# Optimization experiments

Measured on AMD Instinct MI355X. Metric: run time of the kernel, lower is better.

The kernel has to match this reference:

```python
import jax, jax.numpy as jnp
import numpy as np

NEG_SLOPE = 0.01  # torch LeakyReLU default

def leaky_relu(x):
    return jnp.where(x >= 0, x, NEG_SLOPE * x)

def setup_inputs() -> dict:
    key = jax.random.key(0)
    ks = jax.random.split(key, 12)
    D = 128
    N_U, N_I, E = 100000, 50000, 1000000
    s = 1.0 / np.sqrt(D)
    return {
        "h_user": jax.random.normal(ks[0], (N_U, D), jnp.float32),
        "h_item": jax.random.normal(ks[1], (N_I, D), jnp.float32),
        "src_idx": jax.random.randint(ks[2], (E,), 0, N_U, jnp.int64) if jax.config.jax_enable_x64 else jax.random.randint(ks[2], (E,), 0, N_U, jnp.int32),
        "dst_idx": jax.random.randint(ks[3], (E,), 0, N_I, jnp.int32),
        "W_left": jax.random.normal(ks[4], (D, D), jnp.float32) * s,
        "b_left": jax.random.normal(ks[5], (D,), jnp.float32) * s,
        "W_right": jax.random.normal(ks[6], (D, D), jnp.float32) * s,
        "b_right": jax.random.normal(ks[7], (D,), jnp.float32) * s,
        "W1": jax.random.normal(ks[8], (D, D), jnp.float32) * s,
        "b1": jax.random.normal(ks[9], (D,), jnp.float32) * s,
        "W2": jax.random.normal(ks[10], (D, 1), jnp.float32) * s,
        "b2": jax.random.normal(ks[11], (1,), jnp.float32) * s,
    }

def reference(h_user, h_item, src_idx, dst_idx,
              W_left, b_left, W_right, b_right, W1, b1, W2, b2):
    # node linear transforms (dropout is identity in eval mode)
    u_f = h_user @ W_left + b_left      # [N_u, D]
    i_f = h_item @ W_right + b_right    # [N_i, D]
    # edge gather + add (dgl fn.u_add_v)
    score = u_f[src_idx] + i_f[dst_idx]  # [E, D]
    # pred MLP: LeakyReLU -> Linear(D,D) -> LeakyReLU -> Linear(D,1) -> LeakyReLU
    x = leaky_relu(score)
    x = leaky_relu(x @ W1 + b1)
    x = leaky_relu(x @ W2 + b2)         # [E, 1]
    return x
```

## Files before the change

kernel.cpp:

```cpp
#include <hip/hip_runtime.h>

typedef __attribute__((ext_vector_type(8))) short bf16x8;
typedef __attribute__((ext_vector_type(4))) float f32x4;
typedef __attribute__((ext_vector_type(2))) float f32x2;

__device__ __forceinline__ float leaky(float v) { return fmaxf(v, 0.01f * v); }

__device__ __forceinline__ unsigned short f2bf(float a) {
    unsigned int u = __float_as_uint(a);
    return (unsigned short)((u + 0x7FFFu + ((u >> 16) & 1u)) >> 16);
}

__device__ __forceinline__ unsigned int cvtpk(float a, float b) {
#if __has_builtin(__builtin_amdgcn_cvt_pk_bf16_f32)
    typedef __attribute__((ext_vector_type(2))) __bf16 bf2_t;
    bf2_t v = __builtin_amdgcn_cvt_pk_bf16_f32(a, b);
    return __builtin_bit_cast(unsigned int, v);
#else
    unsigned int ua = __float_as_uint(a);
    ua = (ua + 0x7FFFu + ((ua >> 16) & 1u)) >> 16;
    unsigned int ub = __float_as_uint(b);
    ub = (ub + 0x7FFFu + ((ub >> 16) & 1u)) >> 16;
    return ua | (ub << 16);
#endif
}

__device__ __forceinline__ f32x2 unpk2(unsigned int d) {
    f32x2 r;
    r.x = __uint_as_float(d << 16);
    r.y = __uint_as_float(d & 0xFFFF0000u);
    return r;
}

__global__ __launch_bounds__(128) void prep(const float* __restrict__ WL,
                                            const float* __restrict__ WR,
                                            const float* __restrict__ W1,
                                            unsigned short* __restrict__ WLf,
                                            unsigned short* __restrict__ WRf,
                                            unsigned short* __restrict__ Wf) {
    int g = blockIdx.x;
    int f = (g & 127) * 128 + threadIdx.x;
    int j = f & 7, lane = (f >> 3) & 63, nt = (f >> 9) & 7, kb = f >> 12;
    int n = nt * 16 + (lane & 15);
    int kf = kb * 32 + (lane >> 4) * 8 + j;
    if (g < 128) {
        WLf[f] = f2bf(WL[kf * 128 + n]);
    } else if (g < 256) {
        WRf[f] = f2bf(WR[kf * 128 + n]);
    } else {
        int k = (kf & 7) * 16 + (kf >> 3);
        Wf[f] = f2bf(W1[k * 128 + n]);
    }
}

#define PITCH 136

__global__ __launch_bounds__(256, 4) void node_mfma2(const float* __restrict__ h_user,
                                                     const float* __restrict__ h_item,
                                                     const unsigned short* __restrict__ WLf,
                                                     const unsigned short* __restrict__ WRf,
                                                     const float* __restrict__ b_left,
                                                     const float* __restrict__ b_right,
                                                     unsigned short* __restrict__ u_f,
                                                     unsigned short* __restrict__ i_f,
                                                     int N_U, int N_I, int BU) {
    bool isU = (int)blockIdx.x < BU;
    const float* h = isU ? h_user : h_item;
    const unsigned short* Wfr = isU ? WLf : WRf;
    const float* b = isU ? b_left : b_right;
    unsigned short* out = isU ? u_f : i_f;
    int N = isU ? N_U : N_I;
    int r0 = (isU ? blockIdx.x : blockIdx.x - BU) * 128;

    __shared__ unsigned short xt[128 * PITCH];
    int t = threadIdx.x;
    int s = t & 15;
    int el0 = t >> 4;
#pragma unroll
    for (int pass = 0; pass < 8; ++pass) {
        int el = pass * 16 + el0;
        int row = min(r0 + el, N - 1);
        const f32x4* hp = (const f32x4*)(h + (size_t)row * 128);
        f32x4 a0 = hp[s];
        f32x4 a1 = hp[s + 16];
        unsigned int* rp = (unsigned int*)(xt + el * PITCH);
        rp[2 * s]          = cvtpk(a0.x, a0.y);
        rp[2 * s + 1]      = cvtpk(a0.z, a0.w);
        rp[32 + 2 * s]     = cvtpk(a1.x, a1.y);
        rp[32 + 2 * s + 1] = cvtpk(a1.z, a1.w);
    }
    __syncthreads();

    int wave = t >> 6;
    int lane = t & 63;
    int m0 = wave * 32;
    int col = lane & 15;
    int quad = lane >> 4;

    f32x4 acc[2][8];
#pragma unroll
    for (int mt = 0; mt < 2; ++mt)
#pragma unroll
        for (int nt = 0; nt < 8; ++nt) acc[mt][nt] = (f32x4){0.f, 0.f, 0.f, 0.f};

#pragma unroll
    for (int kb = 0; kb < 4; ++kb) {
        bf16x8 afr[2];
#pragma unroll
        for (int mt = 0; mt < 2; ++mt)
            afr[mt] = *(const bf16x8*)(xt + (m0 + mt * 16 + col) * PITCH + kb * 32 + quad * 8);
#pragma unroll
        for (int nt = 0; nt < 8; ++nt) {
            bf16x8 bfr = *(const bf16x8*)(Wfr + ((kb * 8 + nt) * 64 + lane) * 8);
            acc[0][nt] = __builtin_amdgcn_mfma_f32_16x16x32_bf16(afr[0], bfr, acc[0][nt], 0, 0, 0);
            acc[1][nt] = __builtin_amdgcn_mfma_f32_16x16x32_bf16(afr[1], bfr, acc[1][nt], 0, 0, 0);
        }
    }

    float bb[8];
#pragma unroll
    for (int nt = 0; nt < 8; ++nt) bb[nt] = b[nt * 16 + col];
#pragma unroll
    for (int mt = 0; mt < 2; ++mt)
#pragma unroll
        for (int rr = 0; rr < 4; ++rr) {
            int row = r0 + m0 + mt * 16 + quad * 4 + rr;
            uint4 v;
            v.x = cvtpk(acc[mt][0][rr] + bb[0], acc[mt][1][rr] + bb[1]);
            v.y = cvtpk(acc[mt][2][rr] + bb[2], acc[mt][3][rr] + bb[3]);
            v.z = cvtpk(acc[mt][4][rr] + bb[4], acc[mt][5][rr] + bb[5]);
            v.w = cvtpk(acc[mt][6][rr] + bb[6], acc[mt][7][rr] + bb[7]);
            if (row < N) *(uint4*)(out + (size_t)row * 128 + col * 8) = v;
        }
}

#define TE 256

__global__ __launch_bounds__(512, 4) void edge_kernel(
    const unsigned short* __restrict__ u_f, const unsigned short* __restrict__ i_f,
    const int* __restrict__ src, const int* __restrict__ dst,
    const unsigned short* __restrict__ Wf,
    const float* __restrict__ b1, const float* __restrict__ W2,
    const float* __restrict__ b2, float* __restrict__ out, int E) {
    __shared__ unsigned short xt[TE * PITCH];
    __shared__ float zb[4][2][64];
    int t = threadIdx.x;
    int e0 = blockIdx.x * TE;

    int s = t & 15;
    int el0 = t >> 4;
#pragma unroll
    for (int pass = 0; pass < 8; ++pass) {
        int el = pass * 32 + el0;
        int ec = min(e0 + el, E - 1);
        uint4 u4 = *(const uint4*)(u_f + (size_t)src[ec] * 128 + s * 8);
        uint4 i4 = *(const uint4*)(i_f + (size_t)dst[ec] * 128 + s * 8);
        uint4 a;
        {
            f32x2 v;
            v = unpk2(u4.x) + unpk2(i4.x);
            v = __builtin_elementwise_max(v, v * 0.01f);
            a.x = cvtpk(v.x, v.y);
            v = unpk2(u4.y) + unpk2(i4.y);
            v = __builtin_elementwise_max(v, v * 0.01f);
            a.y = cvtpk(v.x, v.y);
            v = unpk2(u4.z) + unpk2(i4.z);
            v = __builtin_elementwise_max(v, v * 0.01f);
            a.z = cvtpk(v.x, v.y);
            v = unpk2(u4.w) + unpk2(i4.w);
            v = __builtin_elementwise_max(v, v * 0.01f);
            a.w = cvtpk(v.x, v.y);
        }
        *(uint4*)(xt + el * PITCH + s * 8) = a;
    }
    __syncthreads();

    int wave = t >> 6;
    int lane = t & 63;
    int col = lane & 15;
    int quad = lane >> 4;
    int wp = wave >> 1;
    int ch = wave & 1;
    int m0 = wp * 64;

    f32x4 acc[4][4];
#pragma unroll
    for (int mt = 0; mt < 4; ++mt)
#pragma unroll
        for (int i = 0; i < 4; ++i) acc[mt][i] = (f32x4){0.f, 0.f, 0.f, 0.f};

#pragma unroll
    for (int kb = 0; kb < 4; ++kb) {
        bf16x8 afr[4];
#pragma unroll
        for (int mt = 0; mt < 4; ++mt)
            afr[mt] = *(const bf16x8*)(xt + (m0 + mt * 16 + col) * PITCH + kb * 32 + quad * 8);
#pragma unroll
        for (int i = 0; i < 4; ++i) {
            int nt = ch * 4 + i;
            bf16x8 bfr = *(const bf16x8*)(Wf + ((kb * 8 + nt) * 64 + lane) * 8);
#pragma unroll
            for (int mt = 0; mt < 4; ++mt)
                acc[mt][i] = __builtin_amdgcn_mfma_f32_16x16x32_bf16(afr[mt], bfr, acc[mt][i], 0, 0, 0);
        }
    }

    f32x4 p[4];
#pragma unroll
    for (int mt = 0; mt < 4; ++mt) p[mt] = (f32x4){0.f, 0.f, 0.f, 0.f};

#pragma unroll
    for (int i = 0; i < 4; ++i) {
        int n = (ch * 4 + i) * 16 + col;
        float bb = b1[n];
        float ww = W2[n];
#pragma unroll
        for (int mt = 0; mt < 4; ++mt) {
            f32x4 y = acc[mt][i] + bb;
            y = __builtin_elementwise_max(y, y * 0.01f);
            p[mt] += y * ww;
        }
    }
#pragma unroll
    for (int off = 1; off < 16; off <<= 1)
#pragma unroll
        for (int mt = 0; mt < 4; ++mt)
#pragma unroll
            for (int rr = 0; rr < 4; ++rr) p[mt][rr] += __shfl_xor(p[mt][rr], off, 64);

    if (col == 0) {
#pragma unroll
        for (int mt = 0; mt < 4; ++mt)
#pragma unroll
            for (int rr = 0; rr < 4; ++rr)
                zb[wp][ch][mt * 16 + quad * 4 + rr] = p[mt][rr];
    }
    __syncthreads();

    if (t < 256) {
        int g = t >> 6;
        int idx = t & 63;
        float z = zb[g][0][idx] + zb[g][1][idx] + b2[0];
        int e = e0 + g * 64 + idx;
        if (e < E) out[e] = leaky(z);
    }
}

extern "C" void kernel_launch(void* const* d_in, const int* in_sizes, int n_in,
                              void* d_out, int out_size, void* d_ws, size_t ws_size,
                              hipStream_t stream) {
    const float* h_user  = (const float*)d_in[0];
    const float* h_item  = (const float*)d_in[1];
    const int*   src_idx = (const int*)d_in[2];
    const int*   dst_idx = (const int*)d_in[3];
    const float* W_left  = (const float*)d_in[4];
    const float* b_left  = (const float*)d_in[5];
    const float* W_right = (const float*)d_in[6];
    const float* b_right = (const float*)d_in[7];
    const float* W1      = (const float*)d_in[8];
    const float* b1      = (const float*)d_in[9];
    const float* W2      = (const float*)d_in[10];
    const float* b2      = (const float*)d_in[11];
    float* out = (float*)d_out;

    int N_U = in_sizes[0] / 128;
    int N_I = in_sizes[1] / 128;
    int E   = in_sizes[2];

    unsigned short* Wf  = (unsigned short*)d_ws;
    unsigned short* WLf = Wf + 16384;
    unsigned short* WRf = WLf + 16384;
    unsigned short* u_f = (unsigned short*)((char*)d_ws + 131072);
    unsigned short* i_f = u_f + (size_t)N_U * 128;

    prep<<<384, 128, 0, stream>>>(W_left, W_right, W1, WLf, WRf, Wf);

    int BU = (N_U + 127) / 128;
    int BI = (N_I + 127) / 128;
    node_mfma2<<<BU + BI, 256, 0, stream>>>(h_user, h_item, WLf, WRf, b_left, b_right,
                                            u_f, i_f, N_U, N_I, BU);

    edge_kernel<<<(E + TE - 1) / TE, 512, 0, stream>>>(u_f, i_f, src_idx, dst_idx,
                                                       Wf, b1, W2, b2, out, E);
}
```

Baseline: 233.8 us.

## Halve edge tile to 128, double occupancy, and batch gather loads before compute

The edge tile shrinks from 256 to 128 edges per 512-thread block, and the launch bound minimum-blocks hint rises from 4 to 8, so more blocks can be resident and LDS per block is halved. The gather phase now issues all four passes of u/i row loads into registers before doing the add/LeakyReLU/convert work, which exposes more memory-level parallelism. The per-wave MFMA work drops to two M-tiles, which lowers register use but halves reuse of each W1 fragment, so W1 is re-read by twice as many blocks.

```diff
diff --git a/kernel.cpp b/kernel.cpp
--- a/kernel.cpp
+++ b/kernel.cpp
@@ -30,6 +30,12 @@
     r.x = __uint_as_float(d << 16);
     r.y = __uint_as_float(d & 0xFFFF0000u);
     return r;
+}
+
+__device__ __forceinline__ unsigned int mix1(unsigned int u, unsigned int i) {
+    f32x2 v = unpk2(u) + unpk2(i);
+    v = __builtin_elementwise_max(v, v * 0.01f);
+    return cvtpk(v.x, v.y);
 }
 
 __global__ __launch_bounds__(128) void prep(const float* __restrict__ WL,
@@ -134,43 +140,37 @@
         }
 }
 
-#define TE 256
-
-__global__ __launch_bounds__(512, 4) void edge_kernel(
+#define TE 128
+
+__global__ __launch_bounds__(512, 8) void edge_kernel(
     const unsigned short* __restrict__ u_f, const unsigned short* __restrict__ i_f,
     const int* __restrict__ src, const int* __restrict__ dst,
     const unsigned short* __restrict__ Wf,
     const float* __restrict__ b1, const float* __restrict__ W2,
     const float* __restrict__ b2, float* __restrict__ out, int E) {
     __shared__ unsigned short xt[TE * PITCH];
-    __shared__ float zb[4][2][64];
+    __shared__ float zb[4][2][32];
     int t = threadIdx.x;
     int e0 = blockIdx.x * TE;
 
     int s = t & 15;
     int el0 = t >> 4;
-#pragma unroll
-    for (int pass = 0; pass < 8; ++pass) {
+
+    uint4 ug[4], ig[4];
+#pragma unroll
+    for (int pass = 0; pass < 4; ++pass) {
+        int ec = min(e0 + pass * 32 + el0, E - 1);
+        ug[pass] = *(const uint4*)(u_f + (size_t)src[ec] * 128 + s * 8);
+        ig[pass] = *(const uint4*)(i_f + (size_t)dst[ec] * 128 + s * 8);
+    }
+#pragma unroll
+    for (int pass = 0; pass < 4; ++pass) {
         int el = pass * 32 + el0;
-        int ec = min(e0 + el, E - 1);
-        uint4 u4 = *(const uint4*)(u_f + (size_t)src[ec] * 128 + s * 8);
-        uint4 i4 = *(const uint4*)(i_f + (size_t)dst[ec] * 128 + s * 8);
         uint4 a;
-        {
-            f32x2 v;
-            v = unpk2(u4.x) + unpk2(i4.x);
-            v = __builtin_elementwise_max(v, v * 0.01f);
-            a.x = cvtpk(v.x, v.y);
-            v = unpk2(u4.y) + unpk2(i4.y);
-            v = __builtin_elementwise_max(v, v * 0.01f);
-            a.y = cvtpk(v.x, v.y);
-            v = unpk2(u4.z) + unpk2(i4.z);
-            v = __builtin_elementwise_max(v, v * 0.01f);
-            a.z = cvtpk(v.x, v.y);
-            v = unpk2(u4.w) + unpk2(i4.w);
-            v = __builtin_elementwise_max(v, v * 0.01f);
-            a.w = cvtpk(v.x, v.y);
-        }
+        a.x = mix1(ug[pass].x, ig[pass].x);
+        a.y = mix1(ug[pass].y, ig[pass].y);
+        a.z = mix1(ug[pass].z, ig[pass].z);
+        a.w = mix1(ug[pass].w, ig[pass].w);
         *(uint4*)(xt + el * PITCH + s * 8) = a;
     }
     __syncthreads();
@@ -181,33 +181,32 @@
     int quad = lane >> 4;
     int wp = wave >> 1;
     int ch = wave & 1;
-    int m0 = wp * 64;
-
-    f32x4 acc[4][4];
-#pragma unroll
-    for (int mt = 0; mt < 4; ++mt)
+    int m0 = wp * 32;
+
+    f32x4 acc[2][4];
+#pragma unroll
+    for (int mt = 0; mt < 2; ++mt)
 #pragma unroll
         for (int i = 0; i < 4; ++i) acc[mt][i] = (f32x4){0.f, 0.f, 0.f, 0.f};
 
 #pragma unroll
     for (int kb = 0; kb < 4; ++kb) {
-        bf16x8 afr[4];
-#pragma unroll
-        for (int mt = 0; mt < 4; ++mt)
+        bf16x8 afr[2];
+#pragma unroll
+        for (int mt = 0; mt < 2; ++mt)
             afr[mt] = *(const bf16x8*)(xt + (m0 + mt * 16 + col) * PITCH + kb * 32 + quad * 8);
 #pragma unroll
         for (int i = 0; i < 4; ++i) {
             int nt = ch * 4 + i;
             bf16x8 bfr = *(const bf16x8*)(Wf + ((kb * 8 + nt) * 64 + lane) * 8);
-#pragma unroll
-            for (int mt = 0; mt < 4; ++mt)
-                acc[mt][i] = __builtin_amdgcn_mfma_f32_16x16x32_bf16(afr[mt], bfr, acc[mt][i], 0, 0, 0);
-        }
-    }
-
-    f32x4 p[4];
-#pragma unroll
-    for (int mt = 0; mt < 4; ++mt) p[mt] = (f32x4){0.f, 0.f, 0.f, 0.f};
+            acc[0][i] = __builtin_amdgcn_mfma_f32_16x16x32_bf16(afr[0], bfr, acc[0][i], 0, 0, 0);
+            acc[1][i] = __builtin_amdgcn_mfma_f32_16x16x32_bf16(afr[1], bfr, acc[1][i], 0, 0, 0);
+        }
+    }
+
+    f32x4 p[2];
+#pragma unroll
+    for (int mt = 0; mt < 2; ++mt) p[mt] = (f32x4){0.f, 0.f, 0.f, 0.f};
 
 #pragma unroll
     for (int i = 0; i < 4; ++i) {
@@ -215,7 +214,7 @@
         float bb = b1[n];
         float ww = W2[n];
 #pragma unroll
-        for (int mt = 0; mt < 4; ++mt) {
+        for (int mt = 0; mt < 2; ++mt) {
             f32x4 y = acc[mt][i] + bb;
             y = __builtin_elementwise_max(y, y * 0.01f);
             p[mt] += y * ww;
@@ -224,24 +223,24 @@
 #pragma unroll
     for (int off = 1; off < 16; off <<= 1)
 #pragma unroll
-        for (int mt = 0; mt < 4; ++mt)
+        for (int mt = 0; mt < 2; ++mt)
 #pragma unroll
             for (int rr = 0; rr < 4; ++rr) p[mt][rr] += __shfl_xor(p[mt][rr], off, 64);
 
     if (col == 0) {
 #pragma unroll
-        for (int mt = 0; mt < 4; ++mt)
+        for (int mt = 0; mt < 2; ++mt)
 #pragma unroll
             for (int rr = 0; rr < 4; ++rr)
                 zb[wp][ch][mt * 16 + quad * 4 + rr] = p[mt][rr];
     }
     __syncthreads();
 
-    if (t < 256) {
-        int g = t >> 6;
-        int idx = t & 63;
+    if (t < 128) {
+        int g = t >> 5;
+        int idx = t & 31;
         float z = zb[g][0][idx] + zb[g][1][idx] + b2[0];
-        int e = e0 + g * 64 + idx;
+        int e = e0 + g * 32 + idx;
         if (e < E) out[e] = leaky(z);
     }
 }
```

Measured after the change: 232.4 us. Within noise of the previous version (-0.6%).
